# Performance work log

Hardware: AMD Instinct MI355X
Metric: run time of the kernel (lower is better)

Reference implementation:

```python
import jax, jax.numpy as jnp
import numpy as np

N_EMBED = 2048
N_HEAD = 16
HEAD_DIM = N_EMBED // N_HEAD
LN_EPS = 1e-5


def setup_inputs() -> dict:
    key = jax.random.key(0)
    ks = jax.random.split(key, 12)
    B, S, D = 4, 2048, N_EMBED
    s = 0.02
    inp = {
        "x": jax.random.normal(ks[0], (B, S, D), jnp.float32),
        "ln1_w": jnp.ones((D,), jnp.float32),
        "ln1_b": jnp.zeros((D,), jnp.float32),
        "Wqkv": jax.random.normal(ks[1], (3 * D, D), jnp.float32) * s,
        "bqkv": jnp.zeros((3 * D,), jnp.float32),
        "Wo": jax.random.normal(ks[2], (D, D), jnp.float32) * s,
        "bo": jnp.zeros((D,), jnp.float32),
        "ln2_w": jnp.ones((D,), jnp.float32),
        "ln2_b": jnp.zeros((D,), jnp.float32),
        "W1": jax.random.normal(ks[3], (4 * D, D), jnp.float32) * s,
        "b1": jnp.zeros((4 * D,), jnp.float32),
        "W2": jax.random.normal(ks[4], (D, 4 * D), jnp.float32) * s,
        "b2": jnp.zeros((D,), jnp.float32),
        # ALiBi slopes: 2^(-8*(h+1)/n_head)
        "slopes": jnp.asarray(2.0 ** (-8.0 * (np.arange(1, N_HEAD + 1)) / N_HEAD), jnp.float32),
    }
    return inp


def layer_norm(x, w, b):
    mu = jnp.mean(x, axis=-1, keepdims=True)
    var = jnp.mean(jnp.square(x - mu), axis=-1, keepdims=True)
    return (x - mu) * jax.lax.rsqrt(var + LN_EPS) * w + b


def attention(h, Wqkv, bqkv, Wo, bo, slopes):
    B, S, D = h.shape
    qkv = jnp.einsum("bsd,ed->bse", h, Wqkv) + bqkv  # [B,S,3D]
    q, k, v = jnp.split(qkv, 3, axis=-1)
    q = q.reshape(B, S, N_HEAD, HEAD_DIM).transpose(0, 2, 1, 3)
    k = k.reshape(B, S, N_HEAD, HEAD_DIM).transpose(0, 2, 1, 3)
    v = v.reshape(B, S, N_HEAD, HEAD_DIM).transpose(0, 2, 1, 3)
    scores = jnp.einsum("bhqd,bhkd->bhqk", q, k) / jnp.sqrt(jnp.float32(HEAD_DIM))
    pos = jnp.arange(S)
    rel = pos[None, :] - pos[:, None]  # j - i, <= 0 on causal part
    alibi = slopes[:, None, None] * rel[None, :, :].astype(jnp.float32)  # [H,S,S]
    causal = rel <= 0
    scores = jnp.where(causal[None, None], scores + alibi[None], -jnp.inf)
    attn = jax.nn.softmax(scores, axis=-1)
    out = jnp.einsum("bhqk,bhkd->bhqd", attn, v)
    out = out.transpose(0, 2, 1, 3).reshape(B, S, D)
    return jnp.einsum("bsd,ed->bse", out, Wo) + bo


def reference(x, ln1_w, ln1_b, Wqkv, bqkv, Wo, bo, ln2_w, ln2_b, W1, b1, W2, b2, slopes):
    # Pre-LN block; dropout in eval mode (identity)
    x = x + attention(layer_norm(x, ln1_w, ln1_b), Wqkv, bqkv, Wo, bo, slopes)
    h = layer_norm(x, ln2_w, ln2_b)
    h = jax.nn.gelu(jnp.einsum("bsd,fd->bsf", h, W1) + b1, approximate=False)
    x = x + jnp.einsum("bsf,df->bsd", h, W2) + b2
    return x
```

## Files before the change

### kernel.cpp

```cpp
#include <hip/hip_runtime.h>

typedef unsigned short ushort_t;
typedef __attribute__((ext_vector_type(8))) short short8;
typedef __attribute__((ext_vector_type(4))) float floatx4;
typedef __attribute__((ext_vector_type(4))) unsigned short ush4;

#define MFMA16x16x32(a, b, c) __builtin_amdgcn_mfma_f32_16x16x32_bf16(a, b, c, 0, 0, 0)

__device__ __forceinline__ float bf2f(ushort_t h) {
    unsigned int u = ((unsigned int)h) << 16;
    return __builtin_bit_cast(float, u);
}
__device__ __forceinline__ ushort_t f2bf(float f) {
    unsigned int u = __builtin_bit_cast(unsigned int, f);
    u += 0x7fffu + ((u >> 16) & 1u);
    return (ushort_t)(u >> 16);
}
__device__ __forceinline__ void gload_lds16(const ushort_t* g, ushort_t* l) {
    __builtin_amdgcn_global_load_lds(
        (const __attribute__((address_space(1))) unsigned int*)g,
        (__attribute__((address_space(3))) unsigned int*)l, 16, 0, 0);
}

__global__ __launch_bounds__(256) void conv_bf16(const float* __restrict__ in,
                                                 ushort_t* __restrict__ out, int n8) {
    int i = blockIdx.x * 256 + threadIdx.x;
    const int stride = gridDim.x * 256;
    for (; i < n8; i += stride) {
        const float* p = in + (size_t)i * 8;
        floatx4 a0 = *(const floatx4*)p;
        floatx4 a1 = *(const floatx4*)(p + 4);
        short8 o;
        o[0] = (short)f2bf(a0[0]); o[1] = (short)f2bf(a0[1]);
        o[2] = (short)f2bf(a0[2]); o[3] = (short)f2bf(a0[3]);
        o[4] = (short)f2bf(a1[0]); o[5] = (short)f2bf(a1[1]);
        o[6] = (short)f2bf(a1[2]); o[7] = (short)f2bf(a1[3]);
        *(short8*)(out + (size_t)i * 8) = o;
    }
}

template <int INF32>
__global__ __launch_bounds__(256) void ln_kernel(const void* __restrict__ in,
                                                 const ushort_t* __restrict__ w,
                                                 const ushort_t* __restrict__ b,
                                                 ushort_t* __restrict__ out) {
    const int row = blockIdx.x;
    const int tid = threadIdx.x;
    const size_t base = (size_t)row * 2048 + (size_t)tid * 8;
    float v[8];
    if (INF32) {
        const float* p = (const float*)in + base;
        floatx4 a0 = *(const floatx4*)p;
        floatx4 a1 = *(const floatx4*)(p + 4);
        v[0] = a0[0]; v[1] = a0[1]; v[2] = a0[2]; v[3] = a0[3];
        v[4] = a1[0]; v[5] = a1[1]; v[6] = a1[2]; v[7] = a1[3];
    } else {
        short8 hv = *(const short8*)((const ushort_t*)in + base);
        const ushort_t* hp = (const ushort_t*)&hv;
#pragma unroll
        for (int k = 0; k < 8; k++) v[k] = bf2f(hp[k]);
    }
    float s = 0.f, sq = 0.f;
#pragma unroll
    for (int k = 0; k < 8; k++) { s += v[k]; sq += v[k] * v[k]; }
#pragma unroll
    for (int m = 32; m; m >>= 1) { s += __shfl_xor(s, m); sq += __shfl_xor(sq, m); }
    __shared__ float red[8];
    const int wv = tid >> 6;
    if ((tid & 63) == 0) { red[wv] = s; red[4 + wv] = sq; }
    __syncthreads();
    s = red[0] + red[1] + red[2] + red[3];
    sq = red[4] + red[5] + red[6] + red[7];
    const float mu = s * (1.f / 2048.f);
    const float var = fmaxf(sq * (1.f / 2048.f) - mu * mu, 0.f);
    const float rs = rsqrtf(var + 1e-5f);
    short8 ov;
#pragma unroll
    for (int k = 0; k < 8; k++) {
        const int c = tid * 8 + k;
        float y = (v[k] - mu) * rs * bf2f(w[c]) + bf2f(b[c]);
        ov[k] = (short)f2bf(y);
    }
    *(short8*)(out + base) = ov;
}

template <int EPI>
__global__ __launch_bounds__(512, 2) void gemm256(const ushort_t* __restrict__ A,
                                                  const ushort_t* __restrict__ W,
                                                  const ushort_t* __restrict__ bias,
                                                  const void* __restrict__ res,
                                                  void* __restrict__ out,
                                                  int M, int N, int K) {
    __shared__ ushort_t smem[65536];
    ushort_t* const As0 = smem;
    ushort_t* const Bs0 = smem + 16384;
    ushort_t* const As1 = smem + 32768;
    ushort_t* const Bs1 = smem + 49152;
    const int tid = threadIdx.x;
    const int lane = tid & 63;
    const int wave = tid >> 6;
    const int la = lane & 15;
    const int qd = lane >> 4;
    const int wrow = (wave >> 2) * 128;
    const int wcol = (wave & 3) * 64;
    const int nbn = N >> 8;
    int bm, bn;
    {
        int wg = (int)blockIdx.x;
        const int cpx = (int)gridDim.x >> 3;
        wg = (wg & 7) * cpx + (wg >> 3);
        const int per = 8 * nbn;
        const int g = wg / per;
        const int rem = wg - g * per;
        bm = g * 8 + (rem & 7);
        bn = rem >> 3;
    }
    const int srow = tid >> 3;
    const int schunk = (tid & 7) ^ (srow & 7);
    const ushort_t* gA = A + (size_t)(bm * 256 + srow) * K + schunk * 8;
    const ushort_t* gB = W + (size_t)(bn * 256 + srow) * K + schunk * 8;
    const int wbase = (tid & ~63) * 8;

    floatx4 acc[8][4];
    const floatx4 z4 = {0.f, 0.f, 0.f, 0.f};
#pragma unroll
    for (int i = 0; i < 8; i++)
#pragma unroll
        for (int j = 0; j < 4; j++) acc[i][j] = z4;
    short8 a[4][2], b[4][2];

#define GBAR()                                    \
    do {                                          \
        asm volatile("" ::: "memory");            \
        __builtin_amdgcn_s_barrier();             \
        asm volatile("" ::: "memory");            \
    } while (0)
#define GLGKM0() asm volatile("s_waitcnt lgkmcnt(0)" ::: "memory")
#define GVM4() asm volatile("s_waitcnt vmcnt(4)" ::: "memory")
#define STG(gp, lb, h, koff)                                                               \
    do {                                                                                   \
        gload_lds16((gp) + (size_t)((h) * 128) * K + (koff), (lb) + ((h) * 128) * 64 + wbase); \
        gload_lds16((gp) + (size_t)((h) * 128 + 64) * K + (koff),                          \
                    (lb) + ((h) * 128 + 64) * 64 + wbase);                                 \
    } while (0)
#define LDA4(base, mh)                                                                     \
    do {                                                                                   \
        _Pragma("unroll") for (int mi = 0; mi < 4; mi++) {                                 \
            const int row_ = wrow + (mh) * 64 + mi * 16 + la;                              \
            a[mi][0] = *(const short8*)&(base)[row_ * 64 + ((qd ^ (la & 7)) * 8)];         \
            a[mi][1] = *(const short8*)&(base)[row_ * 64 + (((4 | qd) ^ (la & 7)) * 8)];   \
        }                                                                                  \
    } while (0)
#define LDB2(base, nl)                                                                     \
    do {                                                                                   \
        _Pragma("unroll") for (int nj = 0; nj < 2; nj++) {                                 \
            const int row_ = wcol + ((nl) + nj) * 16 + la;                                 \
            b[(nl) + nj][0] = *(const short8*)&(base)[row_ * 64 + ((qd ^ (la & 7)) * 8)];  \
            b[(nl) + nj][1] =                                                              \
                *(const short8*)&(base)[row_ * 64 + (((4 | qd) ^ (la & 7)) * 8)];          \
        }                                                                                  \
    } while (0)
#define MMQ(mb, nl)                                                                        \
    do {                                                                                   \
        _Pragma("unroll") for (int ks = 0; ks < 2; ks++)                                   \
            _Pragma("unroll") for (int mi = 0; mi < 4; mi++)                               \
                _Pragma("unroll") for (int nj = 0; nj < 2; nj++) acc[(mb) + mi][(nl) + nj] = \
                    MFMA16x16x32(a[mi][ks], b[(nl) + nj][ks], acc[(mb) + mi][(nl) + nj]);  \
    } while (0)

    const int NT = K >> 6;
    STG(gB, Bs0, 0, 0); STG(gB, Bs0, 1, 0);
    STG(gA, As0, 0, 0); STG(gA, As0, 1, 0);
    STG(gB, Bs1, 0, 64); STG(gB, Bs1, 1, 64);
    GVM4(); GBAR();

    for (int t = 0; t < NT; t += 2) {
        const size_t kA1 = (size_t)(t + 1) * 64;
        const size_t kT2 = (size_t)((t + 2 < NT) ? t + 2 : NT - 1) * 64;
        const size_t kB3 = (size_t)((t + 3 < NT) ? t + 3 : NT - 1) * 64;
        LDA4(As0, 0); LDB2(Bs0, 0); STG(gA, As1, 0, kA1);
        GBAR(); GLGKM0();
        __builtin_amdgcn_s_setprio(1); MMQ(0, 0); __builtin_amdgcn_s_setprio(0);
        GBAR();
        LDB2(Bs0, 2); STG(gA, As1, 1, kA1);
        GBAR(); GLGKM0();
        __builtin_amdgcn_s_setprio(1); MMQ(0, 2); __builtin_amdgcn_s_setprio(0);
        GBAR();
        LDA4(As0, 1); STG(gB, Bs0, 0, kT2);
        GBAR(); GLGKM0();
        __builtin_amdgcn_s_setprio(1); MMQ(4, 2); __builtin_amdgcn_s_setprio(0);
        GBAR();
        STG(gB, Bs0, 1, kT2);
        GBAR();
        __builtin_amdgcn_s_setprio(1); MMQ(4, 0); __builtin_amdgcn_s_setprio(0);
        GVM4(); GBAR();
        LDA4(As1, 0); LDB2(Bs1, 0); STG(gA, As0, 0, kT2);
        GBAR(); GLGKM0();
        __builtin_amdgcn_s_setprio(1); MMQ(0, 0); __builtin_amdgcn_s_setprio(0);
        GBAR();
        LDB2(Bs1, 2); STG(gA, As0, 1, kT2);
        GBAR(); GLGKM0();
        __builtin_amdgcn_s_setprio(1); MMQ(0, 2); __builtin_amdgcn_s_setprio(0);
        GBAR();
        LDA4(As1, 1); STG(gB, Bs1, 0, kB3);
        GBAR(); GLGKM0();
        __builtin_amdgcn_s_setprio(1); MMQ(4, 2); __builtin_amdgcn_s_setprio(0);
        GBAR();
        STG(gB, Bs1, 1, kB3);
        GBAR();
        __builtin_amdgcn_s_setprio(1); MMQ(4, 0); __builtin_amdgcn_s_setprio(0);
        GVM4(); GBAR();
    }
#undef GBAR
#undef GLGKM0
#undef GVM4
#undef STG
#undef LDA4
#undef LDB2
#undef MMQ

    if (EPI == 0) {
        ushort_t* q_out = (ushort_t*)out;
        if (bn < 16) {
            const float qs = (bn < 8) ? (0.08838834764831845f * 1.4426950408889634f) : 1.0f;
            ushort_t* dst = (bn < 8) ? q_out : (q_out + 16777216);
#pragma unroll
            for (int i = 0; i < 8; i++)
#pragma unroll
                for (int j = 0; j < 4; j++)
#pragma unroll
                    for (int r = 0; r < 4; r++) {
                        const int m = bm * 256 + wrow + i * 16 + qd * 4 + r;
                        const int n = bn * 256 + wcol + j * 16 + la;
                        dst[(size_t)m * 2048 + (n & 2047)] =
                            f2bf((acc[i][j][r] + bf2f(bias[n])) * qs);
                    }
        } else {
            ushort_t* v_out = q_out + 33554432;
#pragma unroll
            for (int i = 0; i < 8; i++)
#pragma unroll
                for (int j = 0; j < 4; j++) {
                    const int n = bn * 256 + wcol + j * 16 + la;
                    const int d = n - 4096;
                    const int m0 = bm * 256 + wrow + i * 16 + qd * 4;
                    const int bb = m0 >> 11, s = m0 & 2047;
                    const float bv = bf2f(bias[n]);
                    ush4 pk;
#pragma unroll
                    for (int r = 0; r < 4; r++) pk[r] = f2bf(acc[i][j][r] + bv);
                    *(ush4*)&v_out[((size_t)(bb * 2048 + d)) * 2048 + s] = pk;
                }
        }
    } else {
#pragma unroll
        for (int i = 0; i < 8; i++)
#pragma unroll
            for (int j = 0; j < 4; j++)
#pragma unroll
                for (int r = 0; r < 4; r++) {
                    const int m = bm * 256 + wrow + i * 16 + qd * 4 + r;
                    const int n = bn * 256 + wcol + j * 16 + la;
                    const size_t idx = (size_t)m * N + n;
                    float v = acc[i][j][r] + bf2f(bias[n]);
                    if (EPI == 1) {
                        v += ((const float*)res)[idx];
                        ((ushort_t*)out)[idx] = f2bf(v);
                    } else if (EPI == 2) {
                        v = 0.5f * v * (1.f + erff(v * 0.70710678118654752f));
                        ((ushort_t*)out)[idx] = f2bf(v);
                    } else {
                        v += bf2f(((const ushort_t*)res)[idx]);
                        ((float*)out)[idx] = v;
                    }
                }
    }
}

__global__ __launch_bounds__(256, 2) void attn_kernel(const ushort_t* __restrict__ qb,
                                                      const ushort_t* __restrict__ kb,
                                                      const ushort_t* __restrict__ vtb,
                                                      const float* __restrict__ slopes,
                                                      ushort_t* __restrict__ out) {
    __shared__ ushort_t Ks[16384];
    __shared__ ushort_t Vt[16384];
    __shared__ ushort_t Ps[4096];
    const int tid = threadIdx.x;
    const int lane = tid & 63;
    const int wave = tid >> 6;
    const int la = lane & 15;
    const int qd = lane >> 4;
    const int lid = (int)blockIdx.x;
    const int pair = (lid & 7) * 8 + (lid >> 8);
    const int h = pair & 15;
    const int b = pair >> 4;
    const int qt = 31 - ((lid >> 3) & 31);
    const float slope2 = slopes[h] * 1.4426950408889634f;

    const size_t qrow = (size_t)(b * 2048 + qt * 64 + wave * 16 + la);
    short8 qa[4];
#pragma unroll
    for (int ks = 0; ks < 4; ks++)
        qa[ks] = *(const short8*)&qb[qrow * 2048 + h * 128 + (ks * 4 + qd) * 8];

    const ushort_t* kbase = kb + ((size_t)b * 2048) * 2048 + h * 128;
    const ushort_t* vbase = vtb + ((size_t)(b * 2048 + h * 128)) * 2048;

    floatx4 accO[8];
    const floatx4 z4 = {0.f, 0.f, 0.f, 0.f};
#pragma unroll
    for (int dt = 0; dt < 8; dt++) accO[dt] = z4;
    float mst[4] = {-1e30f, -1e30f, -1e30f, -1e30f};
    float lst[4] = {0.f, 0.f, 0.f, 0.f};

#define AISSUE(kt_, buf_)                                                                   \
    do {                                                                                    \
        _Pragma("unroll") for (int p_ = 0; p_ < 4; p_++) {                                  \
            const int f_ = p_ * 256 + tid;                                                  \
            const int r_ = f_ >> 4;                                                         \
            const int cs_ = f_ & 15;                                                        \
            gload_lds16(kbase + (size_t)((kt_) * 64 + r_) * 2048 + (cs_ ^ (r_ & 15)) * 8,   \
                        Ks + (buf_) * 8192 + (size_t)(p_ * 256 + (tid & ~63)) * 8);         \
        }                                                                                   \
        _Pragma("unroll") for (int p_ = 0; p_ < 4; p_++) {                                  \
            const int f_ = p_ * 256 + tid;                                                  \
            const int d_ = f_ >> 3;                                                         \
            const int c_ = f_ & 7;                                                          \
            gload_lds16(vbase + (size_t)d_ * 2048 + (kt_) * 64 + (c_ ^ (d_ & 7)) * 8,       \
                        Vt + (buf_) * 8192 + (size_t)(p_ * 256 + (tid & ~63)) * 8);         \
        }                                                                                   \
    } while (0)
#define ABAR()                                    \
    do {                                          \
        asm volatile("" ::: "memory");            \
        __builtin_amdgcn_s_barrier();             \
        asm volatile("" ::: "memory");            \
    } while (0)

    AISSUE(0, 0);
    for (int kt = 0; kt <= qt; kt++) {
        const int cur = kt & 1;
        if (kt < qt) {
            AISSUE(kt + 1, cur ^ 1);
            asm volatile("s_waitcnt vmcnt(8)" ::: "memory");
        } else {
            asm volatile("s_waitcnt vmcnt(0)" ::: "memory");
        }
        ABAR();
        const ushort_t* Kc = Ks + cur * 8192;
        const ushort_t* Vc = Vt + cur * 8192;

        floatx4 sc[4];
#pragma unroll
        for (int nt = 0; nt < 4; nt++) sc[nt] = z4;
#pragma unroll
        for (int nt = 0; nt < 4; nt++) {
#pragma unroll
            for (int ks = 0; ks < 4; ks++) {
                short8 kf = *(const short8*)&Kc[(nt * 16 + la) * 128 + ((ks * 4 + qd) ^ la) * 8];
                sc[nt] = MFMA16x16x32(qa[ks], kf, sc[nt]);
            }
        }

        const int knb = kt * 64;
        const bool diag = (kt == qt);
        ushort_t* Pw = Ps + wave * 1024;
        float acol[4];
#pragma unroll
        for (int nt = 0; nt < 4; nt++)
            acol[nt] = slope2 * (float)(knb + nt * 16 + la);
#pragma unroll
        for (int r = 0; r < 4; r++) {
            float rmax = -1e30f;
#pragma unroll
            for (int nt = 0; nt < 4; nt++) {
                float sval = sc[nt][r] + acol[nt];
                if (diag && (nt * 16 + la > wave * 16 + qd * 4 + r)) sval = -1e30f;
                sc[nt][r] = sval;
                rmax = fmaxf(rmax, sval);
            }
            rmax = fmaxf(rmax, __shfl_xor(rmax, 1));
            rmax = fmaxf(rmax, __shfl_xor(rmax, 2));
            rmax = fmaxf(rmax, __shfl_xor(rmax, 4));
            rmax = fmaxf(rmax, __shfl_xor(rmax, 8));
            const float mnew = fmaxf(mst[r], rmax);
            const int row = qd * 4 + r;
            float rsum = 0.f;
#pragma unroll
            for (int nt = 0; nt < 4; nt++) {
                const float pv = __builtin_amdgcn_exp2f(sc[nt][r] - mnew);
                rsum += pv;
                const int col = nt * 16 + la;
                Pw[row * 64 + ((col >> 3) ^ (row & 7)) * 8 + (col & 7)] = f2bf(pv);
            }
            rsum += __shfl_xor(rsum, 1);
            rsum += __shfl_xor(rsum, 2);
            rsum += __shfl_xor(rsum, 4);
            rsum += __shfl_xor(rsum, 8);
            const float alpha = __builtin_amdgcn_exp2f(mst[r] - mnew);
            mst[r] = mnew;
            lst[r] = lst[r] * alpha + rsum;
#pragma unroll
            for (int dt = 0; dt < 8; dt++) accO[dt][r] *= alpha;
        }

#pragma unroll
        for (int k2 = 0; k2 < 2; k2++) {
            short8 pa = *(const short8*)&Pw[la * 64 + ((k2 * 4 + qd) ^ (la & 7)) * 8];
#pragma unroll
            for (int dt = 0; dt < 8; dt++) {
                const int d = dt * 16 + la;
                short8 vf = *(const short8*)&Vc[d * 64 + ((k2 * 4 + qd) ^ (d & 7)) * 8];
                accO[dt] = MFMA16x16x32(pa, vf, accO[dt]);
            }
        }
        ABAR();
    }
#undef AISSUE
#undef ABAR

    const size_t orow0 = (size_t)b * 2048 + qt * 64 + wave * 16 + qd * 4;
#pragma unroll
    for (int r = 0; r < 4; r++) {
        const float inv = 1.f / lst[r];
#pragma unroll
        for (int dt = 0; dt < 8; dt++)
            out[(orow0 + r) * 2048 + h * 128 + dt * 16 + la] = f2bf(accO[dt][r] * inv);
    }
}

extern "C" void kernel_launch(void* const* d_in, const int* in_sizes, int n_in,
                              void* d_out, int out_size, void* d_ws, size_t ws_size,
                              hipStream_t stream) {
    (void)in_sizes; (void)n_in; (void)out_size; (void)ws_size;
    const float* x      = (const float*)d_in[0];
    const float* ln1w   = (const float*)d_in[1];
    const float* ln1b   = (const float*)d_in[2];
    const float* Wqkv   = (const float*)d_in[3];
    const float* bqkv   = (const float*)d_in[4];
    const float* Wo     = (const float*)d_in[5];
    const float* bo     = (const float*)d_in[6];
    const float* ln2w   = (const float*)d_in[7];
    const float* ln2b   = (const float*)d_in[8];
    const float* W1     = (const float*)d_in[9];
    const float* b1     = (const float*)d_in[10];
    const float* W2     = (const float*)d_in[11];
    const float* b2     = (const float*)d_in[12];
    const float* slopes = (const float*)d_in[13];
    float* outp = (float*)d_out;

    char* ws = (char*)d_ws;
    const size_t MB = 1ull << 20;
    ushort_t* wbuf  = (ushort_t*)(ws);
    ushort_t* sv    = (ushort_t*)(ws + 36 * MB);
    ushort_t* ln1w_c = sv;
    ushort_t* ln1b_c = sv + 2048;
    ushort_t* bqkv_c = sv + 4096;
    ushort_t* bo_c   = sv + 10240;
    ushort_t* ln2w_c = sv + 12288;
    ushort_t* ln2b_c = sv + 14336;
    ushort_t* b1_c   = sv + 16384;
    ushort_t* b2_c   = sv + 24576;
    ushort_t* h_buf    = (ushort_t*)(ws + 37 * MB);
    ushort_t* q_buf    = (ushort_t*)(ws + 69 * MB);
    ushort_t* k_buf    = (ushort_t*)(ws + 101 * MB);
    ushort_t* vt_buf   = (ushort_t*)(ws + 133 * MB);
    ushort_t* attn_buf = (ushort_t*)(ws + 165 * MB);
    ushort_t* act_buf  = q_buf;
    ushort_t* x2_buf   = (ushort_t*)(ws + 197 * MB);

    const int M = 8192;

    conv_bf16<<<8, 256, 0, stream>>>(ln1w, ln1w_c, 2048 / 8);
    conv_bf16<<<8, 256, 0, stream>>>(ln1b, ln1b_c, 2048 / 8);
    ln_kernel<1><<<M, 256, 0, stream>>>(x, ln1w_c, ln1b_c, h_buf);
    conv_bf16<<<2048, 256, 0, stream>>>(Wqkv, wbuf, (6144 * 2048) / 8);
    conv_bf16<<<8, 256, 0, stream>>>(bqkv, bqkv_c, 6144 / 8);
    gemm256<0><<<(M / 256) * (6144 / 256), 512, 0, stream>>>(
        h_buf, wbuf, bqkv_c, nullptr, q_buf, M, 6144, 2048);
    attn_kernel<<<2048, 256, 0, stream>>>(q_buf, k_buf, vt_buf, slopes, attn_buf);
    conv_bf16<<<1024, 256, 0, stream>>>(Wo, wbuf, (2048 * 2048) / 8);
    conv_bf16<<<8, 256, 0, stream>>>(bo, bo_c, 2048 / 8);
    gemm256<1><<<(M / 256) * (2048 / 256), 512, 0, stream>>>(
        attn_buf, wbuf, bo_c, x, x2_buf, M, 2048, 2048);
    conv_bf16<<<8, 256, 0, stream>>>(ln2w, ln2w_c, 2048 / 8);
    conv_bf16<<<8, 256, 0, stream>>>(ln2b, ln2b_c, 2048 / 8);
    ln_kernel<0><<<M, 256, 0, stream>>>(x2_buf, ln2w_c, ln2b_c, h_buf);
    conv_bf16<<<2048, 256, 0, stream>>>(W1, wbuf, (8192 * 2048) / 8);
    conv_bf16<<<8, 256, 0, stream>>>(b1, b1_c, 8192 / 8);
    gemm256<2><<<(M / 256) * (8192 / 256), 512, 0, stream>>>(
        h_buf, wbuf, b1_c, nullptr, act_buf, M, 8192, 2048);
    conv_bf16<<<2048, 256, 0, stream>>>(W2, wbuf, (2048 * 8192) / 8);
    conv_bf16<<<8, 256, 0, stream>>>(b2, b2_c, 2048 / 8);
    gemm256<3><<<(M / 256) * (2048 / 256), 512, 0, stream>>>(
        act_buf, wbuf, b2_c, x2_buf, outp, M, 2048, 8192);
}
```

Measured before the change: 1.252 ms.

## Restructure GEMM main loop into four-stage BK=32 LDS pipeline

```diff
diff --git a/kernel.cpp b/kernel.cpp
--- a/kernel.cpp
+++ b/kernel.cpp
@@ -92,10 +92,6 @@
                                                   void* __restrict__ out,
                                                   int M, int N, int K) {
     __shared__ ushort_t smem[65536];
-    ushort_t* const As0 = smem;
-    ushort_t* const Bs0 = smem + 16384;
-    ushort_t* const As1 = smem + 32768;
-    ushort_t* const Bs1 = smem + 49152;
     const int tid = threadIdx.x;
     const int lane = tid & 63;
     const int wave = tid >> 6;
@@ -115,11 +111,12 @@
         bm = g * 8 + (rem & 7);
         bn = rem >> 3;
     }
-    const int srow = tid >> 3;
-    const int schunk = (tid & 7) ^ (srow & 7);
+    const int srow = tid >> 2;
+    const int schunk = (tid & 3) ^ ((srow >> 1) & 3);
     const ushort_t* gA = A + (size_t)(bm * 256 + srow) * K + schunk * 8;
     const ushort_t* gB = W + (size_t)(bn * 256 + srow) * K + schunk * 8;
     const int wbase = (tid & ~63) * 8;
+    const int kch = (qd ^ ((la >> 1) & 3)) * 8;
 
     floatx4 acc[8][4];
     const floatx4 z4 = {0.f, 0.f, 0.f, 0.f};
@@ -127,7 +124,7 @@
     for (int i = 0; i < 8; i++)
 #pragma unroll
         for (int j = 0; j < 4; j++) acc[i][j] = z4;
-    short8 a[4][2], b[4][2];
+    short8 a[4], b[4];
 
 #define GBAR()                                    \
     do {                                          \
@@ -136,88 +133,70 @@
         asm volatile("" ::: "memory");            \
     } while (0)
 #define GLGKM0() asm volatile("s_waitcnt lgkmcnt(0)" ::: "memory")
-#define GVM4() asm volatile("s_waitcnt vmcnt(4)" ::: "memory")
-#define STG(gp, lb, h, koff)                                                               \
-    do {                                                                                   \
-        gload_lds16((gp) + (size_t)((h) * 128) * K + (koff), (lb) + ((h) * 128) * 64 + wbase); \
-        gload_lds16((gp) + (size_t)((h) * 128 + 64) * K + (koff),                          \
-                    (lb) + ((h) * 128 + 64) * 64 + wbase);                                 \
-    } while (0)
-#define LDA4(base, mh)                                                                     \
-    do {                                                                                   \
-        _Pragma("unroll") for (int mi = 0; mi < 4; mi++) {                                 \
-            const int row_ = wrow + (mh) * 64 + mi * 16 + la;                              \
-            a[mi][0] = *(const short8*)&(base)[row_ * 64 + ((qd ^ (la & 7)) * 8)];         \
-            a[mi][1] = *(const short8*)&(base)[row_ * 64 + (((4 | qd) ^ (la & 7)) * 8)];   \
-        }                                                                                  \
-    } while (0)
-#define LDB2(base, nl)                                                                     \
-    do {                                                                                   \
-        _Pragma("unroll") for (int nj = 0; nj < 2; nj++) {                                 \
-            const int row_ = wcol + ((nl) + nj) * 16 + la;                                 \
-            b[(nl) + nj][0] = *(const short8*)&(base)[row_ * 64 + ((qd ^ (la & 7)) * 8)];  \
-            b[(nl) + nj][1] =                                                              \
-                *(const short8*)&(base)[row_ * 64 + (((4 | qd) ^ (la & 7)) * 8)];          \
-        }                                                                                  \
-    } while (0)
-#define MMQ(mb, nl)                                                                        \
-    do {                                                                                   \
-        _Pragma("unroll") for (int ks = 0; ks < 2; ks++)                                   \
-            _Pragma("unroll") for (int mi = 0; mi < 4; mi++)                               \
-                _Pragma("unroll") for (int nj = 0; nj < 2; nj++) acc[(mb) + mi][(nl) + nj] = \
-                    MFMA16x16x32(a[mi][ks], b[(nl) + nj][ks], acc[(mb) + mi][(nl) + nj]);  \
-    } while (0)
-
-    const int NT = K >> 6;
-    STG(gB, Bs0, 0, 0); STG(gB, Bs0, 1, 0);
-    STG(gA, As0, 0, 0); STG(gA, As0, 1, 0);
-    STG(gB, Bs1, 0, 64); STG(gB, Bs1, 1, 64);
-    GVM4(); GBAR();
-
-    for (int t = 0; t < NT; t += 2) {
-        const size_t kA1 = (size_t)(t + 1) * 64;
-        const size_t kT2 = (size_t)((t + 2 < NT) ? t + 2 : NT - 1) * 64;
-        const size_t kB3 = (size_t)((t + 3 < NT) ? t + 3 : NT - 1) * 64;
-        LDA4(As0, 0); LDB2(Bs0, 0); STG(gA, As1, 0, kA1);
-        GBAR(); GLGKM0();
-        __builtin_amdgcn_s_setprio(1); MMQ(0, 0); __builtin_amdgcn_s_setprio(0);
-        GBAR();
-        LDB2(Bs0, 2); STG(gA, As1, 1, kA1);
-        GBAR(); GLGKM0();
-        __builtin_amdgcn_s_setprio(1); MMQ(0, 2); __builtin_amdgcn_s_setprio(0);
-        GBAR();
-        LDA4(As0, 1); STG(gB, Bs0, 0, kT2);
-        GBAR(); GLGKM0();
-        __builtin_amdgcn_s_setprio(1); MMQ(4, 2); __builtin_amdgcn_s_setprio(0);
-        GBAR();
-        STG(gB, Bs0, 1, kT2);
-        GBAR();
-        __builtin_amdgcn_s_setprio(1); MMQ(4, 0); __builtin_amdgcn_s_setprio(0);
-        GVM4(); GBAR();
-        LDA4(As1, 0); LDB2(Bs1, 0); STG(gA, As0, 0, kT2);
-        GBAR(); GLGKM0();
-        __builtin_amdgcn_s_setprio(1); MMQ(0, 0); __builtin_amdgcn_s_setprio(0);
-        GBAR();
-        LDB2(Bs1, 2); STG(gA, As0, 1, kT2);
-        GBAR(); GLGKM0();
-        __builtin_amdgcn_s_setprio(1); MMQ(0, 2); __builtin_amdgcn_s_setprio(0);
-        GBAR();
-        LDA4(As1, 1); STG(gB, Bs1, 0, kB3);
-        GBAR(); GLGKM0();
-        __builtin_amdgcn_s_setprio(1); MMQ(4, 2); __builtin_amdgcn_s_setprio(0);
-        GBAR();
-        STG(gB, Bs1, 1, kB3);
-        GBAR();
-        __builtin_amdgcn_s_setprio(1); MMQ(4, 0); __builtin_amdgcn_s_setprio(0);
-        GVM4(); GBAR();
-    }
+#define GVM8() asm volatile("s_waitcnt vmcnt(8)" ::: "memory")
+#define STGA(koff, b_)                                                                  \
+    do {                                                                                \
+        gload_lds16(gA + (size_t)(koff), smem + (b_)*16384 + wbase);                    \
+        gload_lds16(gA + (size_t)128 * K + (size_t)(koff),                              \
+                    smem + (b_)*16384 + 4096 + wbase);                                  \
+    } while (0)
+#define STGB(koff, b_)                                                                  \
+    do {                                                                                \
+        gload_lds16(gB + (size_t)(koff), smem + (b_)*16384 + 8192 + wbase);             \
+        gload_lds16(gB + (size_t)128 * K + (size_t)(koff),                              \
+                    smem + (b_)*16384 + 12288 + wbase);                                 \
+    } while (0)
+#define LDAF(b_, mh)                                                                    \
+    do {                                                                                \
+        _Pragma("unroll") for (int mi = 0; mi < 4; mi++) {                              \
+            a[mi] = *(const short8*)&smem[(b_)*16384 +                                  \
+                                          (wrow + (mh)*64 + mi * 16 + la) * 32 + kch];  \
+        }                                                                               \
+    } while (0)
+#define LDBF(b_)                                                                        \
+    do {                                                                                \
+        _Pragma("unroll") for (int nj = 0; nj < 4; nj++) {                              \
+            b[nj] = *(const short8*)&smem[(b_)*16384 + 8192 +                           \
+                                          (wcol + nj * 16 + la) * 32 + kch];            \
+        }                                                                               \
+    } while (0)
+#define MM16(mb)                                                                        \
+    do {                                                                                \
+        _Pragma("unroll") for (int mi = 0; mi < 4; mi++)                                \
+            _Pragma("unroll") for (int nj = 0; nj < 4; nj++) acc[(mb) + mi][nj] =       \
+                MFMA16x16x32(a[mi], b[nj], acc[(mb) + mi][nj]);                         \
+    } while (0)
+#define KITER(u)                                                                        \
+    do {                                                                                \
+        const int pre_ = (t + (u) + 3 < NT) ? (t + (u) + 3) : (NT - 1);                 \
+        const size_t ko_ = (size_t)pre_ * 32;                                           \
+        LDAF((u), 0); LDBF((u)); STGA(ko_, ((u) + 3) & 3);                              \
+        GBAR(); GLGKM0();                                                               \
+        __builtin_amdgcn_s_setprio(1); MM16(0); __builtin_amdgcn_s_setprio(0);          \
+        GBAR();                                                                         \
+        LDAF((u), 1); STGB(ko_, ((u) + 3) & 3);                                         \
+        GBAR(); GLGKM0();                                                               \
+        __builtin_amdgcn_s_setprio(1); MM16(4); __builtin_amdgcn_s_setprio(0);          \
+        GVM8(); GBAR();                                                                 \
+    } while (0)
+
+    const int NT = K >> 5;
+    STGA(0, 0); STGB(0, 0);
+    STGA(32, 1); STGB(32, 1);
+    STGA(64, 2); STGB(64, 2);
+    GVM8(); GBAR();
+
+    for (int t = 0; t < NT; t += 4) { KITER(0); KITER(1); KITER(2); KITER(3); }
+    asm volatile("s_waitcnt vmcnt(0)" ::: "memory");
 #undef GBAR
 #undef GLGKM0
-#undef GVM4
-#undef STG
-#undef LDA4
-#undef LDB2
-#undef MMQ
+#undef GVM8
+#undef STGA
+#undef STGB
+#undef LDAF
+#undef LDBF
+#undef MM16
+#undef KITER
 
     if (EPI == 0) {
         ushort_t* q_out = (ushort_t*)out;
```

Result: no change. 1.263 ms (+0.9%).
